# Kernel optimization log

Measured on AMD Instinct MI355X. Metric: run time of the kernel, lower is better.

Reference implementation:

```python
import jax, jax.numpy as jnp
import numpy as np

VOCAB, EMBED, TOPICS, NDOCS = 30000, 200, 100, 2048
DT_ALPHA, TW_ALPHA = 3.0, 2.0
EPS_OT = 1e-16   # ETP sinkhorn epsilon
EPS_LOG = 1e-12  # FASTopic self.epsilon
N_SINKHORN_ITERS = 100  # fixed iteration count (original: while err>thr and cpt<max_iter)


def pairwise_sqeuclidean(x, y):
    return (jnp.sum(x * x, axis=1, keepdims=True)
            + jnp.sum(y * y, axis=1)
            - 2.0 * (x @ y.T))


def sinkhorn_etp(x, y, a, b, alpha):
    # Entropic OT between point clouds x:[n,d], y:[m,d]; a:[n,1], b:[m,1] marginals.
    M = pairwise_sqeuclidean(x, y)          # [n, m]
    K = jnp.exp(-alpha * M)                  # Gibbs kernel
    u0 = jnp.full_like(a, 1.0 / a.shape[0])

    def step(carry, _):
        u, _v = carry
        v = b / (K.T @ u + EPS_OT)           # [m,1]
        u = a / (K @ v + EPS_OT)             # [n,1]
        return (u, v), None

    (u, v), _ = jax.lax.scan(step, (u0, jnp.zeros_like(b)), None, length=N_SINKHORN_ITERS)
    transp = u * (K * v.T)                   # [n, m] transport plan
    loss = jnp.sum(transp * M)
    return loss, transp


def setup_inputs() -> dict:
    key = jax.random.key(0)
    k1, k2, k3, k4 = jax.random.split(key, 4)
    # word_embeddings: trunc_normal(std=1) then L2-row-normalize
    we = jax.random.truncated_normal(k1, -2.0, 2.0, (VOCAB, EMBED), jnp.float32)
    we = we / jnp.linalg.norm(we, axis=1, keepdims=True)
    # topic_embeddings: trunc_normal(std=0.1) then L2-row-normalize
    te = 0.1 * jax.random.truncated_normal(k2, -2.0, 2.0, (TOPICS, EMBED), jnp.float32)
    te = te / jnp.linalg.norm(te, axis=1, keepdims=True)
    word_weights = jnp.full((VOCAB, 1), 1.0 / VOCAB, jnp.float32)
    topic_weights = jnp.full((TOPICS, 1), 1.0 / TOPICS, jnp.float32)
    train_bow = jax.random.uniform(k3, (NDOCS, VOCAB), jnp.float32)
    doc_embeddings = jax.random.normal(k4, (NDOCS, EMBED), jnp.float32)
    return {
        "train_bow": train_bow,
        "doc_embeddings": doc_embeddings,
        "word_embeddings": we,
        "topic_embeddings": te,
        "word_weights": word_weights,
        "topic_weights": topic_weights,
    }


def reference(train_bow, doc_embeddings, word_embeddings, topic_embeddings,
              word_weights, topic_weights):
    n_docs = doc_embeddings.shape[0]
    n_topics = topic_embeddings.shape[0]
    # DT_ETP: a uniform over docs, b = softmax(topic_weights)
    a_dt = jnp.full((n_docs, 1), 1.0 / n_docs, doc_embeddings.dtype)
    b_dt = jax.nn.softmax(topic_weights, axis=0)
    loss_DT, transp_DT = sinkhorn_etp(doc_embeddings, topic_embeddings, a_dt, b_dt, DT_ALPHA)
    # TW_ETP: a uniform over topics, b = softmax(word_weights)
    a_tw = jnp.full((n_topics, 1), 1.0 / n_topics, topic_embeddings.dtype)
    b_tw = jax.nn.softmax(word_weights, axis=0)
    loss_TW, transp_TW = sinkhorn_etp(topic_embeddings, word_embeddings, a_tw, b_tw, TW_ALPHA)

    loss_ETP = loss_DT + loss_TW
    theta = transp_DT * n_docs               # [N, K]
    beta = transp_TW * n_topics              # [K, V]
    recon = theta @ beta                     # [N, V]
    loss_DSR = -jnp.mean(jnp.sum(train_bow * jnp.log(recon + EPS_LOG), axis=1))
    loss = loss_DSR + loss_ETP
    return loss, loss_DSR, loss_ETP
```

## Files before the change

kernel.cpp:

```cpp
#include <hip/hip_runtime.h>
#include <math.h>

#define V 30000
#define E 200
#define T 100
#define N 2048
#define NITER 100
#define KSTR 112
#define EPS_OT 1e-16f
#define EPS_LOG 1e-12f

#define NBTW 40
#define WPT 3
#define NDT 8
#define PSTR 64

#define OFF_KTW    0
#define OFF_KDT    1680000
#define OFF_WW     1884800
#define OFF_DD     1914800
#define OFF_TT     1916848
#define OFF_PM     1916976
#define OFF_PS     1917104
#define OFF_BTW    1917232
#define OFF_BDT    1947232
#define OFF_ACC    1947360
#define OFF_ACCDT  1957360
#define OFF_VTW    1967360
#define OFF_UDT    1997360
#define OFF_UTW    1999408
#define OFF_VDT    1999536
#define OFF_DBL    1999664
#define OFF_FLAG   1999680
#define OFF_KDTNZ  1999681
#define OFF_ARR    1999682
#define OFF_PART   2000000
#define OFF_FLGI   2013000

#define LOBF(u) __uint_as_float((u) << 16)
#define HIBF(u) __uint_as_float((u) & 0xffff0000u)

typedef __attribute__((ext_vector_type(4))) float f32x4;

__device__ __forceinline__ unsigned short f2bf(float f) {
    unsigned int u = __float_as_uint(f);
    return (unsigned short)((u + 0x7fffu + ((u >> 16) & 1u)) >> 16);
}
__device__ __forceinline__ float bf2f(unsigned short h) {
    return __uint_as_float(((unsigned int)h) << 16);
}

__device__ __forceinline__ float brsum(float x, float* red8) {
    int tid = threadIdx.x;
    for (int o = 32; o; o >>= 1) x += __shfl_down(x, o, 64);
    __syncthreads();
    if ((tid & 63) == 0) red8[tid >> 6] = x;
    __syncthreads();
    return (red8[0] + red8[1]) + (red8[2] + red8[3]);
}

__device__ __forceinline__ void load_krow(const unsigned short* kg, int j, unsigned* ku) {
    const uint4* kp = (const uint4*)(kg + (size_t)j * KSTR);
    #pragma unroll
    for (int i = 0; i < 12; i++) {
        uint4 q = kp[i];
        ku[4*i] = q.x; ku[4*i+1] = q.y; ku[4*i+2] = q.z; ku[4*i+3] = q.w;
    }
    uint2 q2 = *(const uint2*)(((const unsigned*)kp) + 48);
    ku[48] = q2.x; ku[49] = q2.y;
}

__device__ __forceinline__ f32x4 ldg_coh4(const float* p) {
    f32x4 r;
    asm volatile("global_load_dwordx4 %0, %1, off sc0 sc1" : "=v"(r) : "v"(p) : "memory");
    return r;
}
__device__ __forceinline__ int ldg_coh1(const int* p) {
    int r;
    asm volatile("global_load_dword %0, %1, off sc0 sc1" : "=v"(r) : "v"(p) : "memory");
    return r;
}
__device__ __forceinline__ void wait_vm0() {
    asm volatile("s_waitcnt vmcnt(0)" ::: "memory");
    __builtin_amdgcn_sched_barrier(0);
}

__device__ __forceinline__ void gbar(int* ctr, int n, int tid) {
    __syncthreads();
    if (tid == 0) {
        __hip_atomic_fetch_add(ctr, 1, __ATOMIC_RELEASE, __HIP_MEMORY_SCOPE_AGENT);
        while (__hip_atomic_load(ctr, __ATOMIC_ACQUIRE, __HIP_MEMORY_SCOPE_AGENT) < n)
            __builtin_amdgcn_s_sleep(1);
    }
    __syncthreads();
}

__device__ __forceinline__ float agent_ldf(const float* p) {
    return __hip_atomic_load(p, __ATOMIC_RELAXED, __HIP_MEMORY_SCOPE_AGENT);
}
__device__ __forceinline__ void agent_stf(float* p, float v) {
    __hip_atomic_store(p, v, __ATOMIC_RELAXED, __HIP_MEMORY_SCOPE_AGENT);
}

__global__ void k_pre(const float* __restrict__ we, const float* __restrict__ de,
                      const float* __restrict__ te, const float* __restrict__ wwgt,
                      const float* __restrict__ twgt, float* ws) {
    __shared__ float red[256];
    int tid = threadIdx.x, b = blockIdx.x;
    int gid = b * 256 + tid;
    if (gid < 2 * NITER * T) ws[OFF_ACC + gid] = 0.f;
    if (gid < 16) ws[OFF_DBL + gid] = 0.f;
    if (gid < 2) ((int*)ws)[OFF_FLAG + gid] = 0;
    if (gid < 2 * NITER) ((int*)ws)[OFF_ARR + gid] = 0;
    if (gid < 640) ((int*)ws)[OFF_FLGI + gid] = 0;
    {
        int r = gid;
        const float* src = nullptr; float* dst = nullptr; int row = 0;
        if (r < V)              { src = we; dst = ws + OFF_WW; row = r; }
        else if (r < V + N)     { src = de; dst = ws + OFF_DD; row = r - V; }
        else if (r < V + N + T) { src = te; dst = ws + OFF_TT; row = r - V - N; }
        if (src) {
            const float4* p = (const float4*)(src + (size_t)row * E);
            float s = 0.f;
            #pragma unroll 10
            for (int i = 0; i < E / 4; i++) { float4 v = p[i]; s += v.x*v.x + v.y*v.y + v.z*v.z + v.w*v.w; }
            dst[row] = s;
        }
    }
    if (b < 118) {
        int j = gid;
        float w = (j < V) ? wwgt[j] : -INFINITY;
        red[tid] = w; __syncthreads();
        for (int s = 128; s > 0; s >>= 1) { if (tid < s) red[tid] = fmaxf(red[tid], red[tid + s]); __syncthreads(); }
        float m = red[0]; __syncthreads();
        float e = (j < V) ? expf(w - m) : 0.f;
        red[tid] = e; __syncthreads();
        for (int s = 128; s > 0; s >>= 1) { if (tid < s) red[tid] += red[tid + s]; __syncthreads(); }
        if (tid == 0) { ws[OFF_PM + b] = m; ws[OFF_PS + b] = red[0]; }
    } else if (b == 120) {
        float w = (tid < T) ? twgt[tid] : -INFINITY;
        red[tid] = w; __syncthreads();
        for (int s = 128; s > 0; s >>= 1) { if (tid < s) red[tid] = fmaxf(red[tid], red[tid + s]); __syncthreads(); }
        float m = red[0]; __syncthreads();
        float e = (tid < T) ? expf(w - m) : 0.f;
        red[tid] = e; __syncthreads();
        for (int s = 128; s > 0; s >>= 1) { if (tid < s) red[tid] += red[tid + s]; __syncthreads(); }
        if (tid < T) ws[OFF_BDT + tid] = e / red[0];
    }
}

__global__ void k_pre2(const float* __restrict__ wwgt, float* ws) {
    __shared__ float red[128];
    int tid = threadIdx.x, b = blockIdx.x;
    float m = (tid < 118) ? ws[OFF_PM + tid] : -INFINITY;
    if (tid < 128) red[tid] = m;
    __syncthreads();
    for (int s = 64; s > 0; s >>= 1) { if (tid < s) red[tid] = fmaxf(red[tid], red[tid + s]); __syncthreads(); }
    float mw = red[0]; __syncthreads();
    float p = (tid < 118) ? ws[OFF_PS + tid] * expf(ws[OFF_PM + tid] - mw) : 0.f;
    if (tid < 128) red[tid] = p;
    __syncthreads();
    for (int s = 64; s > 0; s >>= 1) { if (tid < s) red[tid] += red[tid + s]; __syncthreads(); }
    float Sw = red[0];
    int j = b * 256 + tid;
    if (j < V) ws[OFF_BTW + j] = expf(wwgt[j] - mw) / Sw;
}

__global__ void k_ktw(const float* __restrict__ we, const float* __restrict__ te, float* ws) {
    __shared__ float wt[8][256];
    __shared__ float tp[8][25];
    __shared__ float tts[25];
    int tid = threadIdx.x;
    int j0 = blockIdx.x * 256;
    int t0 = blockIdx.y * 25;
    int j = j0 + tid;
    int jl = (j < V) ? j : V - 1;
    float acc[25];
    #pragma unroll
    for (int i = 0; i < 25; i++) acc[i] = 0.f;
    if (tid < 25) tts[tid] = ws[OFF_TT + t0 + tid];
    for (int kk = 0; kk < E; kk += 8) {
        #pragma unroll
        for (int k = 0; k < 8; k++) wt[k][tid] = we[(size_t)jl * E + kk + k];
        if (tid < 200) { int i = tid >> 3; int k = tid & 7; tp[k][i] = te[(size_t)(t0 + i) * E + kk + k]; }
        __syncthreads();
        #pragma unroll
        for (int k = 0; k < 8; k++) {
            float w = wt[k][tid];
            #pragma unroll
            for (int i = 0; i < 25; i++) acc[i] += tp[k][i] * w;
        }
        __syncthreads();
    }
    if (j < V) {
        float wwj = ws[OFF_WW + j];
        unsigned short* kg = (unsigned short*)(ws + OFF_KTW);
        #pragma unroll
        for (int i = 0; i < 25; i++) {
            float M = tts[i] + wwj - 2.f * acc[i];
            kg[(size_t)j * KSTR + t0 + i] = f2bf(expf(-2.f * M));
        }
    }
}

__global__ void k_kdt(const float* __restrict__ de, const float* __restrict__ te, float* ws) {
    int gid = blockIdx.x * 256 + threadIdx.x;
    if (gid >= N * T) return;
    int n = gid / T; int t = gid - n * T;
    const float4* dp  = (const float4*)(de + (size_t)n * E);
    const float4* tpp = (const float4*)(te + (size_t)t * E);
    float s = 0.f;
    #pragma unroll 10
    for (int i = 0; i < E / 4; i++) { float4 a = dp[i], b = tpp[i]; s += a.x*b.x + a.y*b.y + a.z*b.z + a.w*b.w; }
    float M = ws[OFF_DD + n] + ws[OFF_TT + t] - 2.f * s;
    float kv = expf(-3.f * M);
    ws[OFF_KDT + gid] = kv;
    unsigned long long m = __ballot(kv != 0.f);
    if (m && (threadIdx.x & 63) == 0) atomicOr(((int*)ws) + OFF_KDTNZ, 1);
}

__global__ __launch_bounds__(256, 1) void k_sink(const float* __restrict__ bow, float* ws) {
    __shared__ float sm[256 * 26];
    __shared__ float pr[256];
    __shared__ float u_sh[100];
    __shared__ float red8[8];
    int tid = threadIdx.x, b = blockIdx.x;

    if (b >= NBTW && b < NBTW + 128) {
        const float4* b4 = (const float4*)bow;
        for (int k = 0; k < 96; k++) {
            size_t base = (size_t)k * 160000;
            float s = 0.f;
            for (int i = (b - NBTW) * 256 + tid; i < 160000; i += 128 * 256) {
                float4 x = b4[base + i]; s += (x.x + x.y) + (x.z + x.w);
            }
            float bs = brsum(s, red8);
            if (tid == 0) atomicAdd((double*)(ws + OFF_DBL) + 3, (double)bs);
        }
        return;
    }

    if (b >= NBTW + 128) {
        if (((volatile int*)ws)[OFF_KDTNZ] == 0) return;
        int* arr = ((int*)ws) + OFF_ARR;
        int d = (b - (NBTW + 128)) * 256 + tid;
        const float* Kr = ws + OFF_KDT + (size_t)d * T;
        for (int k = 0; k < NITER; k++) {
            if (tid < T) u_sh[tid] = (k == 0) ? 0.f
                : ws[OFF_BDT + tid] / (agent_ldf(ws + OFF_ACCDT + (k - 1) * T + tid) + EPS_OT);
            __syncthreads();
            float u;
            if (k == 0) u = 1.f / N;
            else {
                float s = 0.f;
                #pragma unroll 4
                for (int t = 0; t < T; t++) s += Kr[t] * u_sh[t];
                u = (1.f / N) / (s + EPS_OT);
            }
            #pragma unroll
            for (int c = 0; c < 4; c++) {
                #pragma unroll
                for (int i = 0; i < 25; i++) sm[tid * 26 + i] = Kr[25 * c + i] * u;
                __syncthreads();
                int g = tid >> 5, tl = tid & 31;
                float s2 = 0.f;
                if (tl < 25) {
                    #pragma unroll 8
                    for (int q = 0; q < 32; q++) s2 += sm[(g * 32 + q) * 26 + tl];
                }
                pr[g * 32 + tl] = s2;
                __syncthreads();
                if (tid < 25) {
                    float r = 0.f;
                    #pragma unroll
                    for (int g2 = 0; g2 < 8; g2++) r += pr[g2 * 32 + tid];
                    atomicAdd(&ws[OFF_ACCDT + k * T + 25 * c + tid], r);
                }
                __syncthreads();
            }
            gbar(arr + NITER + k, NDT, tid);
        }
        if (tid < T) {
            float vf = ws[OFF_BDT + tid] / (agent_ldf(ws + OFF_ACCDT + (NITER - 1) * T + tid) + EPS_OT);
            u_sh[tid] = vf;
            if (b == NBTW + 128) ws[OFF_VDT + tid] = vf;
        }
        __syncthreads();
        float s = 0.f;
        #pragma unroll 4
        for (int t = 0; t < T; t++) s += Kr[t] * u_sh[t];
        float u = (1.f / N) / (s + EPS_OT);
        ws[OFF_UDT + d] = u;
        float ld = 0.f; int nz = 0;
        for (int t = 0; t < T; t++) {
            float kv = Kr[t];
            if (kv > 0.f) ld += u * kv * u_sh[t] * (-(1.f / 3.f) * logf(kv));
            if ((float)N * u * kv * u_sh[t] != 0.f) nz = 1;
        }
        float ldb = brsum(ld, red8);
        if (tid == 0) atomicAdd((double*)(ws + OFF_DBL) + 1, (double)ldb);
        if (nz) atomicOr(((int*)ws) + OFF_FLAG, 1);
        return;
    }

    const unsigned short* kg = (const unsigned short*)(ws + OFF_KTW);
    int* flg = ((int*)ws) + OFF_FLGI;
    unsigned ku[WPT][50];
    float bj[WPT];
    #pragma unroll
    for (int w = 0; w < WPT; w++) {
        int j = (b * WPT + w) * 256 + tid;
        bool oob = (j >= V);
        load_krow(kg, oob ? V - 1 : j, ku[w]);
        if (oob) {
            #pragma unroll
            for (int q = 0; q < 50; q++) ku[w][q] = 0;
        }
        bj[w] = oob ? 0.f : ws[OFF_BTW + j];
    }
    float v[WPT];
    #pragma unroll
    for (int w = 0; w < WPT; w++) v[w] = 0.f;

    for (int k = 0; k < NITER; k++) {
        if (k == 0) {
            if (tid < T) u_sh[tid] = 0.01f;
        } else {
            float rs = 0.f;
            if (tid < 2 * T) {
                int t = tid >> 1, half = tid & 1;
                const float* Pp = ws + OFF_PART + (size_t)((k - 1) & 1) * (T * PSTR)
                                  + t * PSTR + half * 20;
                f32x4 a0 = ldg_coh4(Pp + 0);
                f32x4 a1 = ldg_coh4(Pp + 4);
                f32x4 a2 = ldg_coh4(Pp + 8);
                f32x4 a3 = ldg_coh4(Pp + 12);
                f32x4 a4 = ldg_coh4(Pp + 16);
                wait_vm0();
                rs = (((a0.x + a0.y) + (a0.z + a0.w)) + ((a1.x + a1.y) + (a1.z + a1.w)))
                   + (((a2.x + a2.y) + (a2.z + a2.w)) + ((a3.x + a3.y) + (a3.z + a3.w)))
                   + ((a4.x + a4.y) + (a4.z + a4.w));
            }
            pr[tid] = rs;
            __syncthreads();
            if (tid < T) u_sh[tid] = 0.01f / ((pr[2 * tid] + pr[2 * tid + 1]) + EPS_OT);
        }
        __syncthreads();
        #pragma unroll
        for (int w = 0; w < WPT; w++) {
            float s = 0.f;
            #pragma unroll
            for (int q = 0; q < 50; q++)
                s += LOBF(ku[w][q]) * u_sh[2 * q] + HIBF(ku[w][q]) * u_sh[2 * q + 1];
            v[w] = bj[w] / (s + EPS_OT);
        }
        if (k == NITER - 1) {
            #pragma unroll
            for (int w = 0; w < WPT; w++) {
                int j = (b * WPT + w) * 256 + tid;
                if (j < V) ws[OFF_VTW + j] = v[w];
            }
        }
        float* Pw = ws + OFF_PART + (size_t)(k & 1) * (T * PSTR);
        #pragma unroll
        for (int c = 0; c < 4; c++) {
            #pragma unroll
            for (int i = 0; i < 25; i++) {
                int t = 25 * c + i;
                float p = 0.f;
                #pragma unroll
                for (int w = 0; w < WPT; w++) {
                    unsigned wu = ku[w][t >> 1];
                    float kt = (t & 1) ? HIBF(wu) : LOBF(wu);
                    p += kt * v[w];
                }
                sm[tid * 26 + i] = p;
            }
            __syncthreads();
            int g = tid >> 5, tl = tid & 31;
            float s2 = 0.f;
            if (tl < 25) {
                #pragma unroll 8
                for (int q = 0; q < 32; q++) s2 += sm[(g * 32 + q) * 26 + tl];
            }
            pr[g * 32 + tl] = s2;
            __syncthreads();
            if (tid < 25) {
                float r = 0.f;
                #pragma unroll
                for (int g2 = 0; g2 < 8; g2++) r += pr[g2 * 32 + tid];
                agent_stf(Pw + (25 * c + tid) * PSTR + b, r);
            }
            __syncthreads();
        }
        if (tid == 0)
            __hip_atomic_store(flg + b * 16, k + 1, __ATOMIC_RELEASE, __HIP_MEMORY_SCOPE_AGENT);
        if (tid < 64) {
            const int* fp = flg + (tid < NBTW ? tid : NBTW - 1) * 16;
            while (true) {
                int f = ldg_coh1(fp);
                wait_vm0();
                if (__ballot(f < k + 1) == 0ULL) break;
                __builtin_amdgcn_s_sleep(2);
            }
        }
        __syncthreads();
    }
    {
        float rs = 0.f;
        if (tid < 2 * T) {
            int t = tid >> 1, half = tid & 1;
            const float* Pp = ws + OFF_PART + (size_t)((NITER - 1) & 1) * (T * PSTR)
                              + t * PSTR + half * 20;
            f32x4 a0 = ldg_coh4(Pp + 0);
            f32x4 a1 = ldg_coh4(Pp + 4);
            f32x4 a2 = ldg_coh4(Pp + 8);
            f32x4 a3 = ldg_coh4(Pp + 12);
            f32x4 a4 = ldg_coh4(Pp + 16);
            wait_vm0();
            rs = (((a0.x + a0.y) + (a0.z + a0.w)) + ((a1.x + a1.y) + (a1.z + a1.w)))
               + (((a2.x + a2.y) + (a2.z + a2.w)) + ((a3.x + a3.y) + (a3.z + a3.w)))
               + ((a4.x + a4.y) + (a4.z + a4.w));
        }
        pr[tid] = rs;
        __syncthreads();
        if (tid < T) {
            float uf = 0.01f / ((pr[2 * tid] + pr[2 * tid + 1]) + EPS_OT);
            u_sh[tid] = uf;
            if (b == 0) ws[OFF_UTW + tid] = uf;
        }
    }
    __syncthreads();
    float lt = 0.f;
    #pragma unroll
    for (int w = 0; w < WPT; w++) {
        int j = (b * WPT + w) * 256 + tid;
        if (j < V) {
            #pragma unroll
            for (int q = 0; q < 50; q++) {
                float k0 = LOBF(ku[w][q]), k1 = HIBF(ku[w][q]);
                if (k0 > 0.f) lt += u_sh[2 * q]     * k0 * v[w] * (-0.5f * logf(k0));
                if (k1 > 0.f) lt += u_sh[2 * q + 1] * k1 * v[w] * (-0.5f * logf(k1));
            }
        }
    }
    float ltb = brsum(lt, red8);
    if (tid == 0) atomicAdd((double*)(ws + OFF_DBL) + 2, (double)ltb);
}

__global__ void k_dsr(const float* __restrict__ bow, float* ws) {
    if (*(volatile int*)(((int*)ws) + OFF_FLAG) == 0) return;
    __shared__ float th[32 * T];
    __shared__ float u2[T];
    __shared__ float vd[T];
    __shared__ float red[256];
    __shared__ int flag;
    int tid = threadIdx.x;
    int j0 = blockIdx.x * 256;
    int d0 = blockIdx.y * 32;
    if (tid < T) { vd[tid] = ws[OFF_VDT + tid]; u2[tid] = ws[OFF_UTW + tid]; }
    if (tid == 0) flag = 0;
    __syncthreads();
    bool nz = false;
    for (int idx = tid; idx < 32 * T; idx += 256) {
        int dl = idx / T; int t = idx - dl * T;
        float thv = (float)N * ws[OFF_UDT + d0 + dl] * ws[OFF_KDT + (size_t)(d0 + dl) * T + t] * vd[t];
        th[idx] = thv;
        nz |= (thv != 0.f);
    }
    if (nz) flag = 1;
    __syncthreads();
    int j = j0 + tid;
    float part = 0.f;
    const unsigned short* kg = (const unsigned short*)(ws + OFF_KTW);
    if (flag) {
        float acc[32];
        #pragma unroll
        for (int d = 0; d < 32; d++) acc[d] = 0.f;
        if (j < V) {
            float vj = ws[OFF_VTW + j];
            for (int t = 0; t < T; t++) {
                float kv = bf2f(kg[(size_t)j * KSTR + t]);
                float beta = (float)T * u2[t] * kv * vj;
                #pragma unroll
                for (int d = 0; d < 32; d++) acc[d] += th[d * T + t] * beta;
            }
            for (int d = 0; d < 32; d++)
                part += bow[(size_t)(d0 + d) * V + j] * logf(acc[d] + EPS_LOG);
        }
    } else {
        if (j < V) {
            float sb = 0.f;
            #pragma unroll 8
            for (int d = 0; d < 32; d++) sb += bow[(size_t)(d0 + d) * V + j];
            part = sb * logf(EPS_LOG);
        }
    }
    red[tid] = part; __syncthreads();
    for (int s = 128; s > 0; s >>= 1) { if (tid < s) red[tid] += red[tid + s]; __syncthreads(); }
    if (tid == 0) atomicAdd((double*)(ws + OFF_DBL) + 0, (double)red[0]);
}

__global__ void k_finish(float* ws, float* out) {
    if (threadIdx.x == 0 && blockIdx.x == 0) {
        double* dbl = (double*)(ws + OFF_DBL);
        int flag = ((int*)ws)[OFF_FLAG];
        double dsr_sum = flag ? dbl[0] : dbl[3] * (double)logf(EPS_LOG);
        double ldsr = -dsr_sum / (double)N;
        double letp = dbl[1] + dbl[2];
        out[0] = (float)(ldsr + letp);
        out[1] = (float)ldsr;
        out[2] = (float)letp;
    }
}

extern "C" void kernel_launch(void* const* d_in, const int* in_sizes, int n_in,
                              void* d_out, int out_size, void* d_ws, size_t ws_size,
                              hipStream_t stream) {
    const float* bow  = (const float*)d_in[0];
    const float* de   = (const float*)d_in[1];
    const float* we   = (const float*)d_in[2];
    const float* te   = (const float*)d_in[3];
    const float* wwgt = (const float*)d_in[4];
    const float* twgt = (const float*)d_in[5];
    float* out = (float*)d_out;
    float* ws  = (float*)d_ws;

    k_pre<<<128, 256, 0, stream>>>(we, de, te, wwgt, twgt, ws);
    k_pre2<<<118, 256, 0, stream>>>(wwgt, ws);
    k_ktw<<<dim3(118, 4), 256, 0, stream>>>(we, te, ws);
    k_kdt<<<800, 256, 0, stream>>>(de, te, ws);
    k_sink<<<NBTW + 128 + NDT, 256, 0, stream>>>(bow, ws);
    k_dsr<<<dim3(118, 64), 256, 0, stream>>>(bow, ws);
    k_finish<<<1, 64, 0, stream>>>(ws, out);
}
```

Baseline: 1.350 ms.

## Replace per-iteration flag barrier with sign-tagged partials polled directly

Result: faster. 1.318 ms (-2.4%).

```diff
diff --git a/kernel.cpp b/kernel.cpp
--- a/kernel.cpp
+++ b/kernel.cpp
@@ -35,7 +35,6 @@
 #define OFF_KDTNZ  1999681
 #define OFF_ARR    1999682
 #define OFF_PART   2000000
-#define OFF_FLGI   2013000
 
 #define LOBF(u) __uint_as_float((u) << 16)
 #define HIBF(u) __uint_as_float((u) & 0xffff0000u)
@@ -75,14 +74,47 @@
     asm volatile("global_load_dwordx4 %0, %1, off sc0 sc1" : "=v"(r) : "v"(p) : "memory");
     return r;
 }
-__device__ __forceinline__ int ldg_coh1(const int* p) {
-    int r;
-    asm volatile("global_load_dword %0, %1, off sc0 sc1" : "=v"(r) : "v"(p) : "memory");
-    return r;
+__device__ __forceinline__ void stg_coh1(float* p, float v) {
+    asm volatile("global_store_dword %0, %1, off sc0 sc1" :: "v"(p), "v"(v) : "memory");
 }
 __device__ __forceinline__ void wait_vm0() {
     asm volatile("s_waitcnt vmcnt(0)" ::: "memory");
     __builtin_amdgcn_sched_barrier(0);
+}
+
+__device__ __forceinline__ float poll_sum20(const float* Pp, unsigned ptag) {
+    f32x4 a0, a1, a2, a3, a4;
+    while (true) {
+        a0 = ldg_coh4(Pp + 0);
+        a1 = ldg_coh4(Pp + 4);
+        a2 = ldg_coh4(Pp + 8);
+        a3 = ldg_coh4(Pp + 12);
+        a4 = ldg_coh4(Pp + 16);
+        wait_vm0();
+        unsigned u0x = __float_as_uint(a0.x), u0y = __float_as_uint(a0.y),
+                 u0z = __float_as_uint(a0.z), u0w = __float_as_uint(a0.w);
+        unsigned u1x = __float_as_uint(a1.x), u1y = __float_as_uint(a1.y),
+                 u1z = __float_as_uint(a1.z), u1w = __float_as_uint(a1.w);
+        unsigned u2x = __float_as_uint(a2.x), u2y = __float_as_uint(a2.y),
+                 u2z = __float_as_uint(a2.z), u2w = __float_as_uint(a2.w);
+        unsigned u3x = __float_as_uint(a3.x), u3y = __float_as_uint(a3.y),
+                 u3z = __float_as_uint(a3.z), u3w = __float_as_uint(a3.w);
+        unsigned u4x = __float_as_uint(a4.x), u4y = __float_as_uint(a4.y),
+                 u4z = __float_as_uint(a4.z), u4w = __float_as_uint(a4.w);
+        unsigned and_ = u0x & u0y & u0z & u0w & u1x & u1y & u1z & u1w
+                      & u2x & u2y & u2z & u2w & u3x & u3y & u3z & u3w
+                      & u4x & u4y & u4z & u4w;
+        unsigned or_  = u0x | u0y | u0z | u0w | u1x | u1y | u1z | u1w
+                      | u2x | u2y | u2z | u2w | u3x | u3y | u3z | u3w
+                      | u4x | u4y | u4z | u4w;
+        if (ptag ? (and_ >> 31) : !(or_ >> 31)) break;
+        __builtin_amdgcn_s_sleep(1);
+    }
+    return (((fabsf(a0.x) + fabsf(a0.y)) + (fabsf(a0.z) + fabsf(a0.w)))
+          + ((fabsf(a1.x) + fabsf(a1.y)) + (fabsf(a1.z) + fabsf(a1.w))))
+         + (((fabsf(a2.x) + fabsf(a2.y)) + (fabsf(a2.z) + fabsf(a2.w)))
+          + ((fabsf(a3.x) + fabsf(a3.y)) + (fabsf(a3.z) + fabsf(a3.w))))
+         + ((fabsf(a4.x) + fabsf(a4.y)) + (fabsf(a4.z) + fabsf(a4.w)));
 }
 
 __device__ __forceinline__ void gbar(int* ctr, int n, int tid) {
@@ -97,9 +129,6 @@
 
 __device__ __forceinline__ float agent_ldf(const float* p) {
     return __hip_atomic_load(p, __ATOMIC_RELAXED, __HIP_MEMORY_SCOPE_AGENT);
-}
-__device__ __forceinline__ void agent_stf(float* p, float v) {
-    __hip_atomic_store(p, v, __ATOMIC_RELAXED, __HIP_MEMORY_SCOPE_AGENT);
 }
 
 __global__ void k_pre(const float* __restrict__ we, const float* __restrict__ de,
@@ -112,7 +141,7 @@
     if (gid < 16) ws[OFF_DBL + gid] = 0.f;
     if (gid < 2) ((int*)ws)[OFF_FLAG + gid] = 0;
     if (gid < 2 * NITER) ((int*)ws)[OFF_ARR + gid] = 0;
-    if (gid < 640) ((int*)ws)[OFF_FLGI + gid] = 0;
+    if (gid < 2 * T * PSTR) ws[OFF_PART + gid] = __uint_as_float(0x80000000u);
     {
         int r = gid;
         const float* src = nullptr; float* dst = nullptr; int row = 0;
@@ -304,7 +333,6 @@
     }
 
     const unsigned short* kg = (const unsigned short*)(ws + OFF_KTW);
-    int* flg = ((int*)ws) + OFF_FLGI;
     unsigned ku[WPT][50];
     float bj[WPT];
     #pragma unroll
@@ -331,15 +359,7 @@
                 int t = tid >> 1, half = tid & 1;
                 const float* Pp = ws + OFF_PART + (size_t)((k - 1) & 1) * (T * PSTR)
                                   + t * PSTR + half * 20;
-                f32x4 a0 = ldg_coh4(Pp + 0);
-                f32x4 a1 = ldg_coh4(Pp + 4);
-                f32x4 a2 = ldg_coh4(Pp + 8);
-                f32x4 a3 = ldg_coh4(Pp + 12);
-                f32x4 a4 = ldg_coh4(Pp + 16);
-                wait_vm0();
-                rs = (((a0.x + a0.y) + (a0.z + a0.w)) + ((a1.x + a1.y) + (a1.z + a1.w)))
-                   + (((a2.x + a2.y) + (a2.z + a2.w)) + ((a3.x + a3.y) + (a3.z + a3.w)))
-                   + ((a4.x + a4.y) + (a4.z + a4.w));
+                rs = poll_sum20(Pp, ((k - 1) >> 1) & 1);
             }
             pr[tid] = rs;
             __syncthreads();
@@ -362,6 +382,7 @@
             }
         }
         float* Pw = ws + OFF_PART + (size_t)(k & 1) * (T * PSTR);
+        unsigned wsign = (unsigned)((k >> 1) & 1) << 31;
         #pragma unroll
         for (int c = 0; c < 4; c++) {
             #pragma unroll
@@ -389,22 +410,11 @@
                 float r = 0.f;
                 #pragma unroll
                 for (int g2 = 0; g2 < 8; g2++) r += pr[g2 * 32 + tid];
-                agent_stf(Pw + (25 * c + tid) * PSTR + b, r);
+                stg_coh1(Pw + (25 * c + tid) * PSTR + b,
+                         __uint_as_float(__float_as_uint(r) | wsign));
             }
             __syncthreads();
         }
-        if (tid == 0)
-            __hip_atomic_store(flg + b * 16, k + 1, __ATOMIC_RELEASE, __HIP_MEMORY_SCOPE_AGENT);
-        if (tid < 64) {
-            const int* fp = flg + (tid < NBTW ? tid : NBTW - 1) * 16;
-            while (true) {
-                int f = ldg_coh1(fp);
-                wait_vm0();
-                if (__ballot(f < k + 1) == 0ULL) break;
-                __builtin_amdgcn_s_sleep(2);
-            }
-        }
-        __syncthreads();
     }
     {
         float rs = 0.f;
@@ -412,15 +422,7 @@
             int t = tid >> 1, half = tid & 1;
             const float* Pp = ws + OFF_PART + (size_t)((NITER - 1) & 1) * (T * PSTR)
                               + t * PSTR + half * 20;
-            f32x4 a0 = ldg_coh4(Pp + 0);
-            f32x4 a1 = ldg_coh4(Pp + 4);
-            f32x4 a2 = ldg_coh4(Pp + 8);
-            f32x4 a3 = ldg_coh4(Pp + 12);
-            f32x4 a4 = ldg_coh4(Pp + 16);
-            wait_vm0();
-            rs = (((a0.x + a0.y) + (a0.z + a0.w)) + ((a1.x + a1.y) + (a1.z + a1.w)))
-               + (((a2.x + a2.y) + (a2.z + a2.w)) + ((a3.x + a3.y) + (a3.z + a3.w)))
-               + ((a4.x + a4.y) + (a4.z + a4.w));
+            rs = poll_sum20(Pp, ((NITER - 1) >> 1) & 1);
         }
         pr[tid] = rs;
         __syncthreads();
```
